# Optimization experiments

Measured on AMD Instinct MI355X. Metric: run time of the kernel, lower is better.

The kernel has to match this reference:

```python
import jax, jax.numpy as jnp
import numpy as np

D = 192      # model dim (out_channels)
DIN = 384    # d_inner = 2*D
N = 16       # d_state
DTR = 12     # dt_rank = ceil(D/16)
K = 4        # depthwise conv kernel size
NB = 3       # total mamba blocks (2 stacked + 1 in downsample)


def setup_inputs() -> dict:
    key = jax.random.key(0)
    ks = jax.random.split(key, 8)
    rn = lambda k, shape, s: jax.random.normal(k, shape, jnp.float32) * s
    inp = {
        "x": jax.random.normal(ks[0], (2, 96, 56, 56), jnp.float32),
        "proj_w": rn(ks[1], (D, 96), 0.1),
        "proj_b": jnp.zeros((D,), jnp.float32),
        "bn_g": jnp.ones((D,), jnp.float32),
        "bn_b": jnp.zeros((D,), jnp.float32),
        "bn_mean": jnp.zeros((D,), jnp.float32),
        "bn_var": jnp.ones((D,), jnp.float32),
        "ln_g": jnp.ones((NB, D), jnp.float32),
        "ln_b": jnp.zeros((NB, D), jnp.float32),
        "Win": rn(ks[2], (NB, 2 * DIN, D), 0.05),
        "b_in": jnp.zeros((NB, 2 * DIN), jnp.float32),
        "conv_w": rn(ks[3], (NB, DIN, K), 0.2),
        "conv_b": jnp.zeros((NB, DIN), jnp.float32),
        "Wx": rn(ks[4], (NB, DTR + 2 * N, DIN), 0.05),
        "Wdt": rn(ks[5], (NB, DIN, DTR), 0.05),
        "bdt": jnp.full((NB, DIN), -4.6, jnp.float32),  # softplus ~ 0.01
        "A_log": jnp.log(jnp.broadcast_to(jnp.arange(1, N + 1, dtype=jnp.float32), (NB, DIN, N))),
        "Dskip": jnp.ones((NB, DIN), jnp.float32),
        "Wout": rn(ks[6], (NB, D, DIN), 0.05),
        "bout": jnp.zeros((NB, D), jnp.float32),
    }
    return inp


def _mamba(x, ln_g, ln_b, Win, b_in, conv_w, conv_b, Wx, Wdt, bdt, A_log, Dskip, Wout, bout):
    # x: (B, C, H, W) -> flatten spatial dims to a sequence (B, L, C)
    B, C, H, W = x.shape
    L = H * W
    seq = x.reshape(B, C, L).transpose(0, 2, 1)
    mu = seq.mean(-1, keepdims=True)
    var = seq.var(-1, keepdims=True)
    h = (seq - mu) * jax.lax.rsqrt(var + 1e-5) * ln_g + ln_b  # LayerNorm
    xz = jnp.einsum('bld,ed->ble', h, Win) + b_in              # (B, L, 2*DIN)
    xi, z = jnp.split(xz, 2, axis=-1)
    # depthwise causal conv1d along L
    xc = jnp.pad(xi.transpose(0, 2, 1), ((0, 0), (0, 0), (K - 1, 0)))
    xc = jax.lax.conv_general_dilated(xc, conv_w[:, None, :], (1,), 'VALID',
                                      feature_group_count=DIN) + conv_b[:, None]
    xi = jax.nn.silu(xc).transpose(0, 2, 1)                    # (B, L, DIN)
    proj = jnp.einsum('ble,pe->blp', xi, Wx)                   # (B, L, DTR+2N)
    dtl = proj[..., :DTR]
    Bm = proj[..., DTR:DTR + N]
    Cm = proj[..., DTR + N:]
    dt = jax.nn.softplus(jnp.einsum('blr,er->ble', dtl, Wdt) + bdt)  # (B, L, DIN)
    A = -jnp.exp(A_log)                                         # (DIN, N)
    dA = jnp.exp(dt[..., None] * A)                             # (B, L, DIN, N)
    dBx = (dt * xi)[..., None] * Bm[:, :, None, :]              # (B, L, DIN, N)

    def step(hc, t):
        dA_t, dBx_t, C_t = t
        hc = dA_t * hc + dBx_t                                  # (B, DIN, N)
        return hc, jnp.einsum('ben,bn->be', hc, C_t)

    h0 = jnp.zeros((B, DIN, N), x.dtype)
    _, ys = jax.lax.scan(step, h0, (dA.transpose(1, 0, 2, 3),
                                    dBx.transpose(1, 0, 2, 3),
                                    Cm.transpose(1, 0, 2)))
    y = ys.transpose(1, 0, 2) + Dskip * xi
    y = y * jax.nn.silu(z)
    out = jnp.einsum('ble,de->bld', y, Wout) + bout
    return out.transpose(0, 2, 1).reshape(B, C, H, W)


def _maxpool2(x):
    return jax.lax.reduce_window(x, -jnp.inf, jax.lax.max,
                                 (1, 1, 2, 2), (1, 1, 2, 2), 'VALID')


def reference(x, proj_w, proj_b, bn_g, bn_b, bn_mean, bn_var, ln_g, ln_b, Win, b_in,
              conv_w, conv_b, Wx, Wdt, bdt, A_log, Dskip, Wout, bout):
    # proj (conv1x1) + BatchNorm (eval-mode running stats)
    x = jnp.einsum('bchw,oc->bohw', x, proj_w) + proj_b[:, None, None]
    x = (x - bn_mean[:, None, None]) * jax.lax.rsqrt(bn_var[:, None, None] + 1e-5) \
        * bn_g[:, None, None] + bn_b[:, None, None]
    blk = lambda i, v: _mamba(v, ln_g[i], ln_b[i], Win[i], b_in[i], conv_w[i], conv_b[i],
                              Wx[i], Wdt[i], bdt[i], A_log[i], Dskip[i], Wout[i], bout[i])
    for i in range(2):  # residual mamba blocks
        x = x + blk(i, x)
    skip = x
    x = blk(2, _maxpool2(x))  # downsample: maxpool then mamba (no residual)
    return (x, skip)
```

## Files before the change

### kernel.cpp

```cpp
#include <hip/hip_runtime.h>

typedef __attribute__((ext_vector_type(8))) __bf16 bf16x8;
typedef __attribute__((ext_vector_type(4))) __bf16 bf16x4;
typedef __attribute__((ext_vector_type(4))) float f32x4;

#define DEV static __device__ __forceinline__

DEV float fast_rcp(float x) { return __builtin_amdgcn_rcpf(x); }
DEV float sigm(float x) { return fast_rcp(1.f + __expf(-x)); }
DEV float siluf(float x) { return x * sigm(x); }
DEV float softplusf(float x) { return x > 20.f ? x : __logf(1.f + __expf(x)); }


__global__ __launch_bounds__(256) void k_proj_wcvt(
    const float* __restrict__ x, const float* __restrict__ pw,
    const float* __restrict__ pb, const float* __restrict__ bng,
    const float* __restrict__ bnb, const float* __restrict__ bnm,
    const float* __restrict__ bnv, float* __restrict__ v,
    const float* __restrict__ Win, const float* __restrict__ Wout,
    const float* __restrict__ Wx, __bf16* __restrict__ Wb)
{
  constexpr int SAP = 104;
  __shared__ __bf16 As[64 * SAP];
  __shared__ __bf16 Ws[64 * SAP];
  const int tid = threadIdx.x;
  const int bid = blockIdx.x;

  if (bid >= 294) {
    const int idx = ((bid - 294) * 256 + tid) * 4;
    if (idx < 714240) {
      const float* src;
      if (idx < 442368) src = Win + idx;
      else if (idx < 663552) src = Wout + (idx - 442368);
      else src = Wx + (idx - 663552);
      const float4 tv = *(const float4*)src;
      bf16x4 o;
      o[0] = (__bf16)tv.x; o[1] = (__bf16)tv.y;
      o[2] = (__bf16)tv.z; o[3] = (__bf16)tv.w;
      *(bf16x4*)(Wb + idx) = o;
    }
    return;
  }

  const int r0 = (bid % 98) * 64;
  const int col0 = (bid / 98) * 64;
  const int b = r0 / 3136, l0 = r0 % 3136;
  const int lane = tid & 63, wv = tid >> 6;
  const int rh = wv >> 1, ch = wv & 1;
  const int lm = lane & 15, quad = lane >> 4;

#pragma unroll
  for (int it = 0; it < 6; ++it) {
    const int idx = tid + it * 256;
    const int c = idx >> 4, l4 = idx & 15;
    const float4 t = *(const float4*)(x + ((size_t)(b * 96 + c)) * 3136 + l0 + l4 * 4);
    As[(l4 * 4 + 0) * SAP + c] = (__bf16)t.x;
    As[(l4 * 4 + 1) * SAP + c] = (__bf16)t.y;
    As[(l4 * 4 + 2) * SAP + c] = (__bf16)t.z;
    As[(l4 * 4 + 3) * SAP + c] = (__bf16)t.w;
  }
#pragma unroll
  for (int it = 0; it < 6; ++it) {
    const int idx = tid + it * 256;
    const int wr = idx / 24, kc = (idx % 24) * 4;
    const float4 t = *(const float4*)(pw + (size_t)(col0 + wr) * 96 + kc);
    bf16x4 o;
    o[0] = (__bf16)t.x; o[1] = (__bf16)t.y; o[2] = (__bf16)t.z; o[3] = (__bf16)t.w;
    *(bf16x4*)(&Ws[wr * SAP + kc]) = o;
  }
  __syncthreads();

  f32x4 acc[2][2] = {};
#pragma unroll
  for (int ks = 0; ks < 3; ++ks) {
    const int kb = ks * 32 + quad * 8;
    bf16x8 a0 = *(const bf16x8*)(&As[(rh * 32 + lm) * SAP + kb]);
    bf16x8 a1 = *(const bf16x8*)(&As[(rh * 32 + 16 + lm) * SAP + kb]);
    bf16x8 b0 = *(const bf16x8*)(&Ws[(ch * 32 + lm) * SAP + kb]);
    bf16x8 b1 = *(const bf16x8*)(&Ws[(ch * 32 + 16 + lm) * SAP + kb]);
    acc[0][0] = __builtin_amdgcn_mfma_f32_16x16x32_bf16(a0, b0, acc[0][0], 0, 0, 0);
    acc[0][1] = __builtin_amdgcn_mfma_f32_16x16x32_bf16(a0, b1, acc[0][1], 0, 0, 0);
    acc[1][0] = __builtin_amdgcn_mfma_f32_16x16x32_bf16(a1, b0, acc[1][0], 0, 0, 0);
    acc[1][1] = __builtin_amdgcn_mfma_f32_16x16x32_bf16(a1, b1, acc[1][1], 0, 0, 0);
  }

#pragma unroll
  for (int ti = 0; ti < 2; ++ti)
#pragma unroll
    for (int tj = 0; tj < 2; ++tj) {
      const int gcol = col0 + ch * 32 + tj * 16 + lm;
      const float s = rsqrtf(bnv[gcol] + 1e-5f) * bng[gcol];
      const float sh = (pb[gcol] - bnm[gcol]) * s + bnb[gcol];
#pragma unroll
      for (int j = 0; j < 4; ++j) {
        const int grow = r0 + rh * 32 + ti * 16 + quad * 4 + j;
        v[(size_t)grow * 192 + gcol] = acc[ti][tj][j] * s + sh;
      }
    }
}

__global__ __launch_bounds__(256) void k_conv(
    const float* __restrict__ xz, __bf16* __restrict__ xiB,
    const float* __restrict__ cw, const float* __restrict__ cb,
    int Lseq, int nthreads)
{
  const int idx = blockIdx.x * 256 + threadIdx.x;
  if (idx >= nthreads) return;
  const int e = idx % 384;
  const int seg = idx / 384;
  const int nseg = Lseq / 8;
  const int b = seg / nseg;
  const int l0 = (seg % nseg) * 8;
  const float4 w4 = *(const float4*)(cw + e * 4);
  const float bv = cb[e];
  float xv[11];
#pragma unroll
  for (int k = 0; k < 11; ++k) {
    const int l = l0 - 3 + k;
    xv[k] = (l >= 0) ? xz[(size_t)(b * Lseq + l) * 768 + e] : 0.f;
  }
#pragma unroll
  for (int j = 0; j < 8; ++j) {
    const float a = bv + xv[j] * w4.x + xv[j + 1] * w4.y + xv[j + 2] * w4.z + xv[j + 3] * w4.w;
    xiB[(size_t)(b * Lseq + l0 + j) * 384 + e] = (__bf16)siluf(a);
  }
}

template <int AMODE>
__global__ __launch_bounds__(256, 4) void k_gemm_xz(
    const float* __restrict__ A, const __bf16* __restrict__ W,
    const float* __restrict__ bias, float* __restrict__ O,
    int M, const float* __restrict__ lng, const float* __restrict__ lnb)
{
  constexpr int SA = 200;
  __shared__ __bf16 As[64 * SA];
  __shared__ float lnS[384];
  const int tid = threadIdx.x;
  const int r0 = blockIdx.x * 64;
  const int col0 = blockIdx.y * 128;
  const int lane = tid & 63, wv = tid >> 6;
  const int rh = wv & 1, ch = wv >> 1;
  const int lm = lane & 15, quad = lane >> 4;

  if (tid < 192) { lnS[tid] = lng[tid]; lnS[192 + tid] = lnb[tid]; }
  __syncthreads();

  {
    const int row = tid >> 2, part = tid & 3;
    const int gr = min(r0 + row, M - 1);
    const int cbase = part * 48;
    float4 tv[12];
    if constexpr (AMODE == 2) {
#pragma unroll
      for (int j = 0; j < 12; ++j)
        tv[j] = *(const float4*)(A + (size_t)gr * 192 + cbase + j * 4);
    } else {
      const int bb = gr / 784, l2 = gr % 784;
      const int h2 = l2 / 28, w2 = l2 % 28;
      const float* p0 = A + (size_t)(bb * 3136 + h2 * 112 + w2 * 2) * 192;
#pragma unroll
      for (int j = 0; j < 12; ++j) {
        const int cc = cbase + j * 4;
        const float4 a0 = *(const float4*)(p0 + cc);
        const float4 a1 = *(const float4*)(p0 + 192 + cc);
        const float4 a2 = *(const float4*)(p0 + 56 * 192 + cc);
        const float4 a3 = *(const float4*)(p0 + 57 * 192 + cc);
        tv[j].x = fmaxf(fmaxf(a0.x, a1.x), fmaxf(a2.x, a3.x));
        tv[j].y = fmaxf(fmaxf(a0.y, a1.y), fmaxf(a2.y, a3.y));
        tv[j].z = fmaxf(fmaxf(a0.z, a1.z), fmaxf(a2.z, a3.z));
        tv[j].w = fmaxf(fmaxf(a0.w, a1.w), fmaxf(a2.w, a3.w));
      }
    }
    float s = 0.f, sq = 0.f;
#pragma unroll
    for (int j = 0; j < 12; ++j) {
      s += tv[j].x + tv[j].y + tv[j].z + tv[j].w;
      sq += tv[j].x * tv[j].x + tv[j].y * tv[j].y + tv[j].z * tv[j].z + tv[j].w * tv[j].w;
    }
    s += __shfl_xor(s, 1); s += __shfl_xor(s, 2);
    sq += __shfl_xor(sq, 1); sq += __shfl_xor(sq, 2);
    const float mean = s * (1.f / 192.f);
    const float rstd = rsqrtf(sq * (1.f / 192.f) - mean * mean + 1e-5f);
#pragma unroll
    for (int j = 0; j < 12; ++j) {
      const int c = cbase + j * 4;
      bf16x4 o;
      o[0] = (__bf16)((tv[j].x - mean) * rstd * lnS[c + 0] + lnS[192 + c + 0]);
      o[1] = (__bf16)((tv[j].y - mean) * rstd * lnS[c + 1] + lnS[192 + c + 1]);
      o[2] = (__bf16)((tv[j].z - mean) * rstd * lnS[c + 2] + lnS[192 + c + 2]);
      o[3] = (__bf16)((tv[j].w - mean) * rstd * lnS[c + 3] + lnS[192 + c + 3]);
      *(bf16x4*)(&As[row * SA + c]) = o;
    }
  }
  __syncthreads();

  f32x4 acc[2][4] = {};
#pragma unroll
  for (int ks = 0; ks < 6; ++ks) {
    const int kb = ks * 32 + quad * 8;
    bf16x8 a0 = *(const bf16x8*)(&As[(rh * 32 + lm) * SA + kb]);
    bf16x8 a1 = *(const bf16x8*)(&As[(rh * 32 + 16 + lm) * SA + kb]);
#pragma unroll
    for (int tj = 0; tj < 4; ++tj) {
      const int gw = col0 + ch * 64 + tj * 16 + lm;
      bf16x8 bfr = *(const bf16x8*)(W + (size_t)gw * 192 + kb);
      acc[0][tj] = __builtin_amdgcn_mfma_f32_16x16x32_bf16(a0, bfr, acc[0][tj], 0, 0, 0);
      acc[1][tj] = __builtin_amdgcn_mfma_f32_16x16x32_bf16(a1, bfr, acc[1][tj], 0, 0, 0);
    }
  }

#pragma unroll
  for (int ti = 0; ti < 2; ++ti)
#pragma unroll
    for (int tj = 0; tj < 4; ++tj) {
      const int gcol = col0 + ch * 64 + tj * 16 + lm;
      const float bv = bias[gcol];
#pragma unroll
      for (int j = 0; j < 4; ++j) {
        const int rowt = rh * 32 + ti * 16 + quad * 4 + j;
        const int grow = r0 + rowt;
        if (grow < M) O[(size_t)grow * 768 + gcol] = acc[ti][tj][j] + bv;
      }
    }
}

constexpr int EPI_G2 = 1, EPI_RES = 2, EPI_RES_SKIP = 3, EPI_OUT2 = 4;

template <int EPI>
__global__ __launch_bounds__(256) void k_gemm_s(
    const __bf16* __restrict__ Ab, const __bf16* __restrict__ W,
    const float* __restrict__ bias, float* __restrict__ O,
    int M, int K, int Nvalid,
    float* __restrict__ dtlbuf, float* __restrict__ bcbuf,
    float* __restrict__ oflt)
{
  constexpr int SA = 200;
  __shared__ __align__(16) char smem[16 * SA * 2];
  __bf16* As = (__bf16*)smem;
  __shared__ float dtlS[(EPI == EPI_G2) ? 16 * 12 : 1];
  const int tid = threadIdx.x;
  const int r0 = blockIdx.x * 16;
  const int col0 = blockIdx.y * 64;
  const int lane = tid & 63, wv = tid >> 6;
  const int ch = wv;
  const int lm = lane & 15, quad = lane >> 4;

  f32x4 acc = {};
  const int nkp = K / 192;
  for (int kp = 0; kp < nkp; ++kp) {
    if (kp) __syncthreads();
    {
      const int idx = tid;
      const int row = idx / 24, kc = (idx % 24) * 8;
      const int gr = min(r0 + row, M - 1);
      if (row < 16)
        *(bf16x8*)(&As[row * SA + kc]) =
            *(const bf16x8*)(Ab + (size_t)gr * K + kp * 192 + kc);
      const int idx2 = tid + 256;
      if (idx2 < 384) {
        const int row2 = idx2 / 24, kc2 = (idx2 % 24) * 8;
        const int gr2 = min(r0 + row2, M - 1);
        *(bf16x8*)(&As[row2 * SA + kc2]) =
            *(const bf16x8*)(Ab + (size_t)gr2 * K + kp * 192 + kc2);
      }
    }
    __syncthreads();
#pragma unroll
    for (int ks = 0; ks < 6; ++ks) {
      const int kb = ks * 32 + quad * 8;
      bf16x8 a0 = *(const bf16x8*)(&As[lm * SA + kb]);
      const int gw = min(col0 + ch * 16 + lm, Nvalid - 1);
      bf16x8 bfr = *(const bf16x8*)(W + (size_t)gw * K + kp * 192 + kb);
      acc = __builtin_amdgcn_mfma_f32_16x16x32_bf16(a0, bfr, acc, 0, 0, 0);
    }
  }

  const int colt = ch * 16 + lm;
  if constexpr (EPI == EPI_G2) {
#pragma unroll
    for (int j = 0; j < 4; ++j) {
      const int rowt = quad * 4 + j;
      const int grow = r0 + rowt;
      const float val = acc[j];
      if (colt < 12) dtlS[rowt * 12 + colt] = val;
      else if (colt < 44 && grow < M)
        bcbuf[(size_t)grow * 32 + (colt - 12)] = val;
    }
    __syncthreads();
    if (tid < 192) {
      const int grow = r0 + tid / 12;
      if (grow < M) dtlbuf[(size_t)grow * 12 + tid % 12] = dtlS[tid];
    }
  } else {
    const int gcol = col0 + colt;
    const float bv = bias[gcol];
    float nv4[4];
#pragma unroll
    for (int j = 0; j < 4; ++j) {
      const int rowt = quad * 4 + j;
      const int grow = r0 + rowt;
      const float val = acc[j] + bv;
      if constexpr (EPI == EPI_RES) {
        O[(size_t)grow * 192 + gcol] += val;
      } else if constexpr (EPI == EPI_RES_SKIP) {
        const float nvv = O[(size_t)grow * 192 + gcol] + val;
        O[(size_t)grow * 192 + gcol] = nvv;
        nv4[j] = nvv;
      } else {
        nv4[j] = val;
      }
    }
    if constexpr (EPI == EPI_RES_SKIP || EPI == EPI_OUT2) {
      float* tS = (float*)smem;
      __syncthreads();
#pragma unroll
      for (int j = 0; j < 4; ++j)
        tS[(quad * 4 + j) * 66 + colt] = nv4[j];
      __syncthreads();
      constexpr int Lpix = (EPI == EPI_RES_SKIP) ? 3136 : 784;
      constexpr int strideB = (EPI == EPI_RES_SKIP) ? 602112 : 150528;
      const int c2 = tid >> 2, part = tid & 3;
      const int bb = r0 / Lpix;
      const int l0 = r0 - bb * Lpix;
      float4 o4;
      o4.x = tS[(part * 4 + 0) * 66 + c2];
      o4.y = tS[(part * 4 + 1) * 66 + c2];
      o4.z = tS[(part * 4 + 2) * 66 + c2];
      o4.w = tS[(part * 4 + 3) * 66 + c2];
      *(float4*)(oflt + (size_t)bb * strideB + (size_t)(col0 + c2) * Lpix +
                 l0 + part * 4) = o4;
    }
  }
}

constexpr int SC_LC = 14;

__global__ __launch_bounds__(256) void k_scan1(
    const float* __restrict__ dtl, const __bf16* __restrict__ xi,
    const float* __restrict__ bc, const float* __restrict__ Wdt,
    const float* __restrict__ bdt, const float* __restrict__ A_log,
    float* __restrict__ DT, float* __restrict__ S, int Lseq, int NC)
{
  __shared__ float Bs[SC_LC * 16];
  __shared__ float dts[SC_LC * 128];
  __shared__ float dtlS[SC_LC * 12];
  __shared__ float wdtS[12 * 128];
  const int t = threadIdx.x;
  const int el = t >> 1, half = t & 1, n0h = half * 8;
  const int e0 = blockIdx.y * 128;
  const int e = e0 + el;
  const int c = blockIdx.x % NC;
  const int b = blockIdx.x / NC;
  const int rowbase = b * Lseq + c * SC_LC;

  if (t < SC_LC * 16)
    Bs[t] = bc[(size_t)(rowbase + (t >> 4)) * 32 + (t & 15)];
  if (t < SC_LC * 12)
    dtlS[t] = dtl[(size_t)(rowbase + t / 12) * 12 + t % 12];
  for (int idx = t; idx < 12 * 128; idx += 256) {
    const int r = idx >> 7, ee = idx & 127;
    wdtS[idx] = Wdt[(size_t)(e0 + ee) * 12 + r];
  }
  const float bdte = bdt[e];

  float An2[8];
  {
    const float4* a4 = (const float4*)(A_log + e * 16 + n0h);
    float4 t0 = a4[0], t1 = a4[1];
    float tmp[8] = {t0.x, t0.y, t0.z, t0.w, t1.x, t1.y, t1.z, t1.w};
#pragma unroll
    for (int n = 0; n < 8; ++n) An2[n] = -__expf(tmp[n]) * 1.44269504f;
  }
  __syncthreads();
  float dtp = 0.f;
#pragma unroll
  for (int j = 0; j < 7; ++j) {
    const int l = half * 7 + j;
    float a = bdte;
#pragma unroll
    for (int r = 0; r < 12; ++r) a += dtlS[l * 12 + r] * wdtS[r * 128 + el];
    const float sp = softplusf(a);
    dts[l * 128 + el] = sp;
    dtp += sp;
  }
  const float dtsum = dtp + __shfl_xor(dtp, 1);
  __syncthreads();

  float xall[SC_LC];
#pragma unroll
  for (int l = 0; l < SC_LC; ++l)
    xall[l] = (float)xi[(size_t)(rowbase + l) * 384 + e];

  float h[8];
#pragma unroll
  for (int n = 0; n < 8; ++n) h[n] = 0.f;
#pragma unroll
  for (int l = 0; l < SC_LC; ++l) {
    const float dtv = dts[l * 128 + el];
    const float u = dtv * xall[l];
    const float* Brow = &Bs[l * 16 + n0h];
#pragma unroll
    for (int n = 0; n < 8; ++n) {
      const float a = __builtin_amdgcn_exp2f(dtv * An2[n]);
      h[n] = a * h[n] + u * Brow[n];
    }
  }
  const size_t o = ((size_t)(b * NC + c) * 384 + e) * 16 + n0h;
  *(float4*)(S + o)     = make_float4(h[0], h[1], h[2], h[3]);
  *(float4*)(S + o + 4) = make_float4(h[4], h[5], h[6], h[7]);
  if (half == 0) DT[(size_t)(b * NC + c) * 384 + e] = dtsum;
}

__global__ __launch_bounds__(256) void k_carry(
    const float* __restrict__ DT, float* __restrict__ SH,
    const float* __restrict__ A_log, int NC)
{
  const int tid = blockIdx.x * 256 + threadIdx.x;
  const int b = tid / 6144, r = tid % 6144;
  const float An2 = -__expf(A_log[r]) * 1.44269504f;
  const size_t o = (size_t)b * NC * 6144 + r;
  const size_t od = (size_t)b * NC * 384 + (r >> 4);

  float sA[8], dA[8], sB[8], dB[8];
  auto LOAD = [&](float (&sv)[8], float (&dv)[8], int c0) {
#pragma unroll
    for (int k = 0; k < 8; ++k) {
      sv[k] = SH[o + (size_t)(c0 + k) * 6144];
      dv[k] = DT[od + (size_t)(c0 + k) * 384];
    }
  };
  float h = 0.f;
  auto COMP = [&](const float (&sv)[8], const float (&dv)[8], int c0) {
    float a[8];
#pragma unroll
    for (int k = 0; k < 8; ++k) a[k] = __builtin_amdgcn_exp2f(An2 * dv[k]);
#pragma unroll
    for (int k = 0; k < 8; ++k) {
      SH[o + (size_t)(c0 + k) * 6144] = h;
      h = a[k] * h + sv[k];
    }
  };

  LOAD(sA, dA, 0);
  for (int c0 = 0; c0 < NC; c0 += 16) {
    if (c0 + 8 < NC) LOAD(sB, dB, c0 + 8);
    COMP(sA, dA, c0);
    if (c0 + 8 < NC) {
      if (c0 + 16 < NC) LOAD(sA, dA, c0 + 16);
      COMP(sB, dB, c0 + 8);
    }
  }
}

__global__ __launch_bounds__(256) void k_scan2(
    const float* __restrict__ dtl, const __bf16* __restrict__ xi,
    const float* __restrict__ bc, const float* __restrict__ xz,
    const float* __restrict__ Wdt, const float* __restrict__ bdt,
    const float* __restrict__ A_log, const float* __restrict__ Dskip,
    const float* __restrict__ H0, __bf16* __restrict__ y, int Lseq, int NC)
{
  __shared__ float BCs[SC_LC * 32];
  __shared__ float dts[SC_LC * 128];
  __shared__ float dtlS[SC_LC * 12];
  __shared__ float wdtS[12 * 128];
  const int t = threadIdx.x;
  const int el = t >> 1, half = t & 1, n0h = half * 8;
  const int e0 = blockIdx.y * 128;
  const int e = e0 + el;
  const int c = blockIdx.x % NC;
  const int b = blockIdx.x / NC;
  const int rowbase = b * Lseq + c * SC_LC;

  for (int idx = t; idx < SC_LC * 32; idx += 256)
    BCs[idx] = bc[(size_t)rowbase * 32 + idx];
  if (t < SC_LC * 12)
    dtlS[t] = dtl[(size_t)(rowbase + t / 12) * 12 + t % 12];
  for (int idx = t; idx < 12 * 128; idx += 256) {
    const int r = idx >> 7, ee = idx & 127;
    wdtS[idx] = Wdt[(size_t)(e0 + ee) * 12 + r];
  }
  const float bdte = bdt[e];

  float An2[8];
  {
    const float4* a4 = (const float4*)(A_log + e * 16 + n0h);
    float4 t0 = a4[0], t1 = a4[1];
    float tmp[8] = {t0.x, t0.y, t0.z, t0.w, t1.x, t1.y, t1.z, t1.w};
#pragma unroll
    for (int n = 0; n < 8; ++n) An2[n] = -__expf(tmp[n]) * 1.44269504f;
  }
  float h[8];
  {
    const size_t o = ((size_t)(b * NC + c) * 384 + e) * 16 + n0h;
    const float4* h4 = (const float4*)(H0 + o);
    float4 t0 = h4[0], t1 = h4[1];
    h[0]=t0.x; h[1]=t0.y; h[2]=t0.z; h[3]=t0.w;
    h[4]=t1.x; h[5]=t1.y; h[6]=t1.z; h[7]=t1.w;
  }
  __syncthreads();
#pragma unroll
  for (int j = 0; j < 7; ++j) {
    const int l = half * 7 + j;
    float a = bdte;
#pragma unroll
    for (int r = 0; r < 12; ++r) a += dtlS[l * 12 + r] * wdtS[r * 128 + el];
    dts[l * 128 + el] = softplusf(a);
  }
  __syncthreads();
  const float Dse = Dskip[e];

  float xall[SC_LC], zall[SC_LC];
#pragma unroll
  for (int l = 0; l < SC_LC; ++l) {
    const size_t r = (size_t)(rowbase + l);
    xall[l] = (float)xi[r * 384 + e];
    zall[l] = xz[r * 768 + 384 + e];
  }

#pragma unroll
  for (int l = 0; l < SC_LC; ++l) {
    const float dtv = dts[l * 128 + el];
    const float xiv = xall[l];
    const float u = dtv * xiv;
    const float* Brow = &BCs[l * 32 + n0h];
    const float* Crow = &BCs[l * 32 + 16 + n0h];
    float yv = 0.f;
#pragma unroll
    for (int n = 0; n < 8; ++n) {
      const float a = __builtin_amdgcn_exp2f(dtv * An2[n]);
      h[n] = a * h[n] + u * Brow[n];
      yv += h[n] * Crow[n];
    }
    const float yt = yv + __shfl_xor(yv, 1);
    if (half == 0)
      y[(size_t)(rowbase + l) * 384 + e] = (__bf16)((yt + Dse * xiv) * siluf(zall[l]));
  }
}

extern "C" void kernel_launch(void* const* d_in, const int* in_sizes, int n_in,
                              void* d_out, int out_size, void* d_ws, size_t ws_size,
                              hipStream_t stream)
{
  const float* x    = (const float*)d_in[0];
  const float* pw   = (const float*)d_in[1];
  const float* pb   = (const float*)d_in[2];
  const float* bng  = (const float*)d_in[3];
  const float* bnb  = (const float*)d_in[4];
  const float* bnm  = (const float*)d_in[5];
  const float* bnv  = (const float*)d_in[6];
  const float* lng  = (const float*)d_in[7];
  const float* lnb  = (const float*)d_in[8];
  const float* Win  = (const float*)d_in[9];
  const float* b_in = (const float*)d_in[10];
  const float* cw   = (const float*)d_in[11];
  const float* cb   = (const float*)d_in[12];
  const float* Wx   = (const float*)d_in[13];
  const float* Wdt  = (const float*)d_in[14];
  const float* bdt  = (const float*)d_in[15];
  const float* Alog = (const float*)d_in[16];
  const float* Dsk  = (const float*)d_in[17];
  const float* Wout = (const float*)d_in[18];
  const float* bout = (const float*)d_in[19];

  float* wsf = (float*)d_ws;
  float* v    = wsf;
  float* xz   = v + 1204224;
  float* dtlb = xz + 4816896;
  float* bcb  = dtlb + 75264;
  float* Sb   = bcb + 200704;
  float* Pb   = Sb + 2752512;
  __bf16* xiB = (__bf16*)(Pb + 2752512);
  __bf16* yB  = (__bf16*)(Pb + 2752512 + 1204224);
  __bf16* Wb  = (__bf16*)(Pb + 2752512 + 2408448);

  float* out0 = (float*)d_out;
  float* out1 = out0 + 301056;

  k_proj_wcvt<<<992, 256, 0, stream>>>(x, pw, pb, bng, bnb, bnm, bnv, v,
                                       Win, Wout, Wx, Wb);

  for (int i = 0; i < 3; ++i) {
    const int big = (i < 2) ? 1 : 0;
    const int Lseq = big ? 3136 : 784;
    const int M = 2 * Lseq;
    const int NC = Lseq / SC_LC;
    const int MB = (M + 63) / 64;
    const int MB16 = M / 16;
    const float* lng_i = lng + i * 192;
    const float* lnb_i = lnb + i * 192;
    const float* bin_i = b_in + i * 768;
    const float* cw_i  = cw + i * 384 * 4;
    const float* cb_i  = cb + i * 384;
    const float* Wdt_i = Wdt + i * 384 * 12;
    const float* bdt_i = bdt + i * 384;
    const float* Al_i  = Alog + i * 384 * 16;
    const float* Ds_i  = Dsk + i * 384;
    const float* bo_i  = bout + i * 192;
    const __bf16* Winb_i  = Wb + i * 147456;
    const __bf16* Woutb_i = Wb + 442368 + i * 73728;
    const __bf16* Wxb_i   = Wb + 663552 + i * 16896;

    if (big)
      k_gemm_xz<2><<<dim3(MB, 6), 256, 0, stream>>>(
          v, Winb_i, bin_i, xz, M, lng_i, lnb_i);
    else
      k_gemm_xz<3><<<dim3(MB, 6), 256, 0, stream>>>(
          v, Winb_i, bin_i, xz, M, lng_i, lnb_i);
    k_conv<<<(M * 384 / 8 + 255) / 256, 256, 0, stream>>>(
        xz, xiB, cw_i, cb_i, Lseq, M * 384 / 8);
    k_gemm_s<EPI_G2><<<dim3(MB16, 1), 256, 0, stream>>>(
        xiB, Wxb_i, nullptr, nullptr, M, 384, 44, dtlb, bcb, nullptr);
    k_scan1<<<dim3(2 * NC, 3), 256, 0, stream>>>(
        dtlb, xiB, bcb, Wdt_i, bdt_i, Al_i, Pb, Sb, Lseq, NC);
    k_carry<<<48, 256, 0, stream>>>(Pb, Sb, Al_i, NC);
    k_scan2<<<dim3(2 * NC, 3), 256, 0, stream>>>(
        dtlb, xiB, bcb, xz, Wdt_i, bdt_i, Al_i, Ds_i, Sb, yB, Lseq, NC);
    if (i == 0)
      k_gemm_s<EPI_RES><<<dim3(MB16, 3), 256, 0, stream>>>(
          yB, Woutb_i, bo_i, v, M, 384, 192, nullptr, nullptr, nullptr);
    else if (i == 1)
      k_gemm_s<EPI_RES_SKIP><<<dim3(MB16, 3), 256, 0, stream>>>(
          yB, Woutb_i, bo_i, v, M, 384, 192, nullptr, nullptr, out1);
    else
      k_gemm_s<EPI_OUT2><<<dim3(MB16, 3), 256, 0, stream>>>(
          yB, Woutb_i, bo_i, v, M, 384, 192, nullptr, nullptr, out0);
  }
}
```

Measured before the change: 328.1 us.

## Fuse x_proj GEMM into both scan kernels, recomputing dt/B/C per chunk

Removes the separate x_proj GEMM launch (dt-low-rank, B, C) and instead computes the 14-row x 44-column projection with MFMA inside k_scan1 and k_scan2, from xi rows staged in shared memory. The staged xi tile is also reused for the per-channel x values, and the dts buffer aliases the staging area. This saves one launch per block and the global round trip for dtl/bc. In exchange the projection is computed twice and redundantly across the three channel-group blocks. Each 16-row MFMA tile also carries 2 wasted rows, which adds LDS pressure to the scan kernels.

```diff
diff --git a/kernel.cpp b/kernel.cpp
--- a/kernel.cpp
+++ b/kernel.cpp
@@ -224,20 +224,17 @@
     }
 }
 
-constexpr int EPI_G2 = 1, EPI_RES = 2, EPI_RES_SKIP = 3, EPI_OUT2 = 4;
+constexpr int EPI_RES = 2, EPI_RES_SKIP = 3, EPI_OUT2 = 4;
 
 template <int EPI>
 __global__ __launch_bounds__(256) void k_gemm_s(
     const __bf16* __restrict__ Ab, const __bf16* __restrict__ W,
     const float* __restrict__ bias, float* __restrict__ O,
-    int M, int K, int Nvalid,
-    float* __restrict__ dtlbuf, float* __restrict__ bcbuf,
-    float* __restrict__ oflt)
+    int M, int K, int Nvalid, float* __restrict__ oflt)
 {
   constexpr int SA = 200;
   __shared__ __align__(16) char smem[16 * SA * 2];
   __bf16* As = (__bf16*)smem;
-  __shared__ float dtlS[(EPI == EPI_G2) ? 16 * 12 : 1];
   const int tid = threadIdx.x;
   const int r0 = blockIdx.x * 16;
   const int col0 = blockIdx.y * 64;
@@ -276,75 +273,61 @@
   }
 
   const int colt = ch * 16 + lm;
-  if constexpr (EPI == EPI_G2) {
-#pragma unroll
-    for (int j = 0; j < 4; ++j) {
-      const int rowt = quad * 4 + j;
-      const int grow = r0 + rowt;
-      const float val = acc[j];
-      if (colt < 12) dtlS[rowt * 12 + colt] = val;
-      else if (colt < 44 && grow < M)
-        bcbuf[(size_t)grow * 32 + (colt - 12)] = val;
-    }
+  const int gcol = col0 + colt;
+  const float bv = bias[gcol];
+  float nv4[4];
+#pragma unroll
+  for (int j = 0; j < 4; ++j) {
+    const int rowt = quad * 4 + j;
+    const int grow = r0 + rowt;
+    const float val = acc[j] + bv;
+    if constexpr (EPI == EPI_RES) {
+      O[(size_t)grow * 192 + gcol] += val;
+    } else if constexpr (EPI == EPI_RES_SKIP) {
+      const float nvv = O[(size_t)grow * 192 + gcol] + val;
+      O[(size_t)grow * 192 + gcol] = nvv;
+      nv4[j] = nvv;
+    } else {
+      nv4[j] = val;
+    }
+  }
+  if constexpr (EPI == EPI_RES_SKIP || EPI == EPI_OUT2) {
+    float* tS = (float*)smem;
     __syncthreads();
-    if (tid < 192) {
-      const int grow = r0 + tid / 12;
-      if (grow < M) dtlbuf[(size_t)grow * 12 + tid % 12] = dtlS[tid];
-    }
-  } else {
-    const int gcol = col0 + colt;
-    const float bv = bias[gcol];
-    float nv4[4];
-#pragma unroll
-    for (int j = 0; j < 4; ++j) {
-      const int rowt = quad * 4 + j;
-      const int grow = r0 + rowt;
-      const float val = acc[j] + bv;
-      if constexpr (EPI == EPI_RES) {
-        O[(size_t)grow * 192 + gcol] += val;
-      } else if constexpr (EPI == EPI_RES_SKIP) {
-        const float nvv = O[(size_t)grow * 192 + gcol] + val;
-        O[(size_t)grow * 192 + gcol] = nvv;
-        nv4[j] = nvv;
-      } else {
-        nv4[j] = val;
-      }
-    }
-    if constexpr (EPI == EPI_RES_SKIP || EPI == EPI_OUT2) {
-      float* tS = (float*)smem;
-      __syncthreads();
-#pragma unroll
-      for (int j = 0; j < 4; ++j)
-        tS[(quad * 4 + j) * 66 + colt] = nv4[j];
-      __syncthreads();
-      constexpr int Lpix = (EPI == EPI_RES_SKIP) ? 3136 : 784;
-      constexpr int strideB = (EPI == EPI_RES_SKIP) ? 602112 : 150528;
-      const int c2 = tid >> 2, part = tid & 3;
-      const int bb = r0 / Lpix;
-      const int l0 = r0 - bb * Lpix;
-      float4 o4;
-      o4.x = tS[(part * 4 + 0) * 66 + c2];
-      o4.y = tS[(part * 4 + 1) * 66 + c2];
-      o4.z = tS[(part * 4 + 2) * 66 + c2];
-      o4.w = tS[(part * 4 + 3) * 66 + c2];
-      *(float4*)(oflt + (size_t)bb * strideB + (size_t)(col0 + c2) * Lpix +
-                 l0 + part * 4) = o4;
-    }
+#pragma unroll
+    for (int j = 0; j < 4; ++j)
+      tS[(quad * 4 + j) * 66 + colt] = nv4[j];
+    __syncthreads();
+    constexpr int Lpix = (EPI == EPI_RES_SKIP) ? 3136 : 784;
+    constexpr int strideB = (EPI == EPI_RES_SKIP) ? 602112 : 150528;
+    const int c2 = tid >> 2, part = tid & 3;
+    const int bb = r0 / Lpix;
+    const int l0 = r0 - bb * Lpix;
+    float4 o4;
+    o4.x = tS[(part * 4 + 0) * 66 + c2];
+    o4.y = tS[(part * 4 + 1) * 66 + c2];
+    o4.z = tS[(part * 4 + 2) * 66 + c2];
+    o4.w = tS[(part * 4 + 3) * 66 + c2];
+    *(float4*)(oflt + (size_t)bb * strideB + (size_t)(col0 + c2) * Lpix +
+               l0 + part * 4) = o4;
   }
 }
 
 constexpr int SC_LC = 14;
 
 __global__ __launch_bounds__(256) void k_scan1(
-    const float* __restrict__ dtl, const __bf16* __restrict__ xi,
-    const float* __restrict__ bc, const float* __restrict__ Wdt,
-    const float* __restrict__ bdt, const float* __restrict__ A_log,
+    const __bf16* __restrict__ xi, const __bf16* __restrict__ Wx,
+    const float* __restrict__ Wdt, const float* __restrict__ bdt,
+    const float* __restrict__ A_log,
     float* __restrict__ DT, float* __restrict__ S, int Lseq, int NC)
 {
-  __shared__ float Bs[SC_LC * 16];
-  __shared__ float dts[SC_LC * 128];
+  constexpr int SA = 200;
+  __shared__ __align__(16) char asmem[2 * 16 * SA * 2];
+  __shared__ float BCs[SC_LC * 32];
   __shared__ float dtlS[SC_LC * 12];
   __shared__ float wdtS[12 * 128];
+  __bf16* As = (__bf16*)asmem;
+  float* dts = (float*)asmem;
   const int t = threadIdx.x;
   const int el = t >> 1, half = t & 1, n0h = half * 8;
   const int e0 = blockIdx.y * 128;
@@ -352,17 +335,31 @@
   const int c = blockIdx.x % NC;
   const int b = blockIdx.x / NC;
   const int rowbase = b * Lseq + c * SC_LC;
-
-  if (t < SC_LC * 16)
-    Bs[t] = bc[(size_t)(rowbase + (t >> 4)) * 32 + (t & 15)];
-  if (t < SC_LC * 12)
-    dtlS[t] = dtl[(size_t)(rowbase + t / 12) * 12 + t % 12];
+  const int M2 = 2 * Lseq;
+  const int lane = t & 63, wv = t >> 6;
+  const int lm = lane & 15, quad = lane >> 4;
+
+#pragma unroll
+  for (int kp = 0; kp < 2; ++kp) {
+    const int row = t / 24, kc = (t % 24) * 8;
+    if (row < 16) {
+      const int gr = min(rowbase + row, M2 - 1);
+      *(bf16x8*)(&As[kp * 16 * SA + row * SA + kc]) =
+          *(const bf16x8*)(xi + (size_t)gr * 384 + kp * 192 + kc);
+    }
+    const int idx2 = t + 256;
+    if (idx2 < 384) {
+      const int row2 = idx2 / 24, kc2 = (idx2 % 24) * 8;
+      const int gr2 = min(rowbase + row2, M2 - 1);
+      *(bf16x8*)(&As[kp * 16 * SA + row2 * SA + kc2]) =
+          *(const bf16x8*)(xi + (size_t)gr2 * 384 + kp * 192 + kc2);
+    }
+  }
   for (int idx = t; idx < 12 * 128; idx += 256) {
     const int r = idx >> 7, ee = idx & 127;
     wdtS[idx] = Wdt[(size_t)(e0 + ee) * 12 + r];
   }
   const float bdte = bdt[e];
-
   float An2[8];
   {
     const float4* a4 = (const float4*)(A_log + e * 16 + n0h);
@@ -372,6 +369,40 @@
     for (int n = 0; n < 8; ++n) An2[n] = -__expf(tmp[n]) * 1.44269504f;
   }
   __syncthreads();
+
+  f32x4 acc = {};
+#pragma unroll
+  for (int kp = 0; kp < 2; ++kp)
+#pragma unroll
+    for (int ks = 0; ks < 6; ++ks) {
+      const int kb = ks * 32 + quad * 8;
+      bf16x8 a0 = *(const bf16x8*)(&As[kp * 16 * SA + lm * SA + kb]);
+      const int gw = min(wv * 16 + lm, 43);
+      bf16x8 bfr = *(const bf16x8*)(Wx + (size_t)gw * 384 + kp * 192 + kb);
+      acc = __builtin_amdgcn_mfma_f32_16x16x32_bf16(a0, bfr, acc, 0, 0, 0);
+    }
+  float xall[SC_LC];
+  {
+    const int kp = e >= 192, col = e - kp * 192;
+#pragma unroll
+    for (int l = 0; l < SC_LC; ++l)
+      xall[l] = (float)As[kp * 16 * SA + l * SA + col];
+  }
+  __syncthreads();
+
+  {
+    const int colt = wv * 16 + lm;
+#pragma unroll
+    for (int j = 0; j < 4; ++j) {
+      const int rowt = quad * 4 + j;
+      if (rowt < SC_LC) {
+        if (colt < 12) dtlS[rowt * 12 + colt] = acc[j];
+        else if (colt < 44) BCs[rowt * 32 + (colt - 12)] = acc[j];
+      }
+    }
+  }
+  __syncthreads();
+
   float dtp = 0.f;
 #pragma unroll
   for (int j = 0; j < 7; ++j) {
@@ -386,11 +417,6 @@
   const float dtsum = dtp + __shfl_xor(dtp, 1);
   __syncthreads();
 
-  float xall[SC_LC];
-#pragma unroll
-  for (int l = 0; l < SC_LC; ++l)
-    xall[l] = (float)xi[(size_t)(rowbase + l) * 384 + e];
-
   float h[8];
 #pragma unroll
   for (int n = 0; n < 8; ++n) h[n] = 0.f;
@@ -398,7 +424,7 @@
   for (int l = 0; l < SC_LC; ++l) {
     const float dtv = dts[l * 128 + el];
     const float u = dtv * xall[l];
-    const float* Brow = &Bs[l * 16 + n0h];
+    const float* Brow = &BCs[l * 32 + n0h];
 #pragma unroll
     for (int n = 0; n < 8; ++n) {
       const float a = __builtin_amdgcn_exp2f(dtv * An2[n]);
@@ -453,16 +479,19 @@
 }
 
 __global__ __launch_bounds__(256) void k_scan2(
-    const float* __restrict__ dtl, const __bf16* __restrict__ xi,
-    const float* __restrict__ bc, const float* __restrict__ xz,
-    const float* __restrict__ Wdt, const float* __restrict__ bdt,
-    const float* __restrict__ A_log, const float* __restrict__ Dskip,
-    const float* __restrict__ H0, __bf16* __restrict__ y, int Lseq, int NC)
-{
+    const __bf16* __restrict__ xi, const __bf16* __restrict__ Wx,
+    const float* __restrict__ xz, const float* __restrict__ Wdt,
+    const float* __restrict__ bdt, const float* __restrict__ A_log,
+    const float* __restrict__ Dskip, const float* __restrict__ H0,
+    __bf16* __restrict__ y, int Lseq, int NC)
+{
+  constexpr int SA = 200;
+  __shared__ __align__(16) char asmem[2 * 16 * SA * 2];
   __shared__ float BCs[SC_LC * 32];
-  __shared__ float dts[SC_LC * 128];
   __shared__ float dtlS[SC_LC * 12];
   __shared__ float wdtS[12 * 128];
+  __bf16* As = (__bf16*)asmem;
+  float* dts = (float*)asmem;
   const int t = threadIdx.x;
   const int el = t >> 1, half = t & 1, n0h = half * 8;
   const int e0 = blockIdx.y * 128;
@@ -470,17 +499,31 @@
   const int c = blockIdx.x % NC;
   const int b = blockIdx.x / NC;
   const int rowbase = b * Lseq + c * SC_LC;
-
-  for (int idx = t; idx < SC_LC * 32; idx += 256)
-    BCs[idx] = bc[(size_t)rowbase * 32 + idx];
-  if (t < SC_LC * 12)
-    dtlS[t] = dtl[(size_t)(rowbase + t / 12) * 12 + t % 12];
+  const int M2 = 2 * Lseq;
+  const int lane = t & 63, wv = t >> 6;
+  const int lm = lane & 15, quad = lane >> 4;
+
+#pragma unroll
+  for (int kp = 0; kp < 2; ++kp) {
+    const int row = t / 24, kc = (t % 24) * 8;
+    if (row < 16) {
+      const int gr = min(rowbase + row, M2 - 1);
+      *(bf16x8*)(&As[kp * 16 * SA + row * SA + kc]) =
+          *(const bf16x8*)(xi + (size_t)gr * 384 + kp * 192 + kc);
+    }
+    const int idx2 = t + 256;
+    if (idx2 < 384) {
+      const int row2 = idx2 / 24, kc2 = (idx2 % 24) * 8;
+      const int gr2 = min(rowbase + row2, M2 - 1);
+      *(bf16x8*)(&As[kp * 16 * SA + row2 * SA + kc2]) =
+          *(const bf16x8*)(xi + (size_t)gr2 * 384 + kp * 192 + kc2);
+    }
+  }
   for (int idx = t; idx < 12 * 128; idx += 256) {
     const int r = idx >> 7, ee = idx & 127;
     wdtS[idx] = Wdt[(size_t)(e0 + ee) * 12 + r];
   }
   const float bdte = bdt[e];
-
   float An2[8];
   {
     const float4* a4 = (const float4*)(A_log + e * 16 + n0h);
@@ -497,7 +540,45 @@
     h[0]=t0.x; h[1]=t0.y; h[2]=t0.z; h[3]=t0.w;
     h[4]=t1.x; h[5]=t1.y; h[6]=t1.z; h[7]=t1.w;
   }
-  __syncthreads();
+  float zall[SC_LC];
+#pragma unroll
+  for (int l = 0; l < SC_LC; ++l)
+    zall[l] = xz[(size_t)(rowbase + l) * 768 + 384 + e];
+  __syncthreads();
+
+  f32x4 acc = {};
+#pragma unroll
+  for (int kp = 0; kp < 2; ++kp)
+#pragma unroll
+    for (int ks = 0; ks < 6; ++ks) {
+      const int kb = ks * 32 + quad * 8;
+      bf16x8 a0 = *(const bf16x8*)(&As[kp * 16 * SA + lm * SA + kb]);
+      const int gw = min(wv * 16 + lm, 43);
+      bf16x8 bfr = *(const bf16x8*)(Wx + (size_t)gw * 384 + kp * 192 + kb);
+      acc = __builtin_amdgcn_mfma_f32_16x16x32_bf16(a0, bfr, acc, 0, 0, 0);
+    }
+  float xall[SC_LC];
+  {
+    const int kp = e >= 192, col = e - kp * 192;
+#pragma unroll
+    for (int l = 0; l < SC_LC; ++l)
+      xall[l] = (float)As[kp * 16 * SA + l * SA + col];
+  }
+  __syncthreads();
+
+  {
+    const int colt = wv * 16 + lm;
+#pragma unroll
+    for (int j = 0; j < 4; ++j) {
+      const int rowt = quad * 4 + j;
+      if (rowt < SC_LC) {
+        if (colt < 12) dtlS[rowt * 12 + colt] = acc[j];
+        else if (colt < 44) BCs[rowt * 32 + (colt - 12)] = acc[j];
+      }
+    }
+  }
+  __syncthreads();
+
 #pragma unroll
   for (int j = 0; j < 7; ++j) {
     const int l = half * 7 + j;
@@ -508,14 +589,6 @@
   }
   __syncthreads();
   const float Dse = Dskip[e];
-
-  float xall[SC_LC], zall[SC_LC];
-#pragma unroll
-  for (int l = 0; l < SC_LC; ++l) {
-    const size_t r = (size_t)(rowbase + l);
-    xall[l] = (float)xi[r * 384 + e];
-    zall[l] = xz[r * 768 + 384 + e];
-  }
 
 #pragma unroll
   for (int l = 0; l < SC_LC; ++l) {
@@ -608,21 +681,19 @@
           v, Winb_i, bin_i, xz, M, lng_i, lnb_i);
     k_conv<<<(M * 384 / 8 + 255) / 256, 256, 0, stream>>>(
         xz, xiB, cw_i, cb_i, Lseq, M * 384 / 8);
-    k_gemm_s<EPI_G2><<<dim3(MB16, 1), 256, 0, stream>>>(
-        xiB, Wxb_i, nullptr, nullptr, M, 384, 44, dtlb, bcb, nullptr);
     k_scan1<<<dim3(2 * NC, 3), 256, 0, stream>>>(
-        dtlb, xiB, bcb, Wdt_i, bdt_i, Al_i, Pb, Sb, Lseq, NC);
+        xiB, Wxb_i, Wdt_i, bdt_i, Al_i, Pb, Sb, Lseq, NC);
     k_carry<<<48, 256, 0, stream>>>(Pb, Sb, Al_i, NC);
     k_scan2<<<dim3(2 * NC, 3), 256, 0, stream>>>(
-        dtlb, xiB, bcb, xz, Wdt_i, bdt_i, Al_i, Ds_i, Sb, yB, Lseq, NC);
+        xiB, Wxb_i, xz, Wdt_i, bdt_i, Al_i, Ds_i, Sb, yB, Lseq, NC);
     if (i == 0)
       k_gemm_s<EPI_RES><<<dim3(MB16, 3), 256, 0, stream>>>(
-          yB, Woutb_i, bo_i, v, M, 384, 192, nullptr, nullptr, nullptr);
+          yB, Woutb_i, bo_i, v, M, 384, 192, nullptr);
     else if (i == 1)
       k_gemm_s<EPI_RES_SKIP><<<dim3(MB16, 3), 256, 0, stream>>>(
-          yB, Woutb_i, bo_i, v, M, 384, 192, nullptr, nullptr, out1);
+          yB, Woutb_i, bo_i, v, M, 384, 192, out1);
     else
       k_gemm_s<EPI_OUT2><<<dim3(MB16, 3), 256, 0, stream>>>(
-          yB, Woutb_i, bo_i, v, M, 384, 192, nullptr, nullptr, out0);
-  }
-}
+          yB, Woutb_i, bo_i, v, M, 384, 192, out0);
+  }
+}
```

Result: slower. 337.9 us (+3.0%).
